# Performance work log

Measured on AMD Instinct MI355X. Metric: run time of the kernel, lower is better.

## Reference

```python
import jax, jax.numpy as jnp
import numpy as np
import math

N_NODES = 20000
N_EDGES = 320000
NODE_IN = 128
HIDDEN = 64
HEADS = 4
TIME_DIM = 64
SCALE = 60.0 / 1.0  # sensitivity / epsilon


def _linear_params(key, din, dout):
    k1, k2 = jax.random.split(key)
    bound = 1.0 / math.sqrt(din)
    w = jax.random.uniform(k1, (din, dout), minval=-bound, maxval=bound, dtype=jnp.float32)
    b = jax.random.uniform(k2, (dout,), minval=-bound, maxval=bound, dtype=jnp.float32)
    return w, b


def setup_inputs() -> dict:
    key = jax.random.key(0)
    ks = jax.random.split(key, 16)
    edge_index = jax.random.randint(ks[0], (2, N_EDGES), 0, N_NODES, dtype=jnp.int64)
    raw_time = jax.random.uniform(ks[1], (N_EDGES, 1), dtype=jnp.float32) * 86400.0
    noise = jax.random.laplace(ks[2], (N_EDGES, 1), dtype=jnp.float32) * SCALE
    node_emb = jax.random.normal(ks[3], (N_NODES, NODE_IN), dtype=jnp.float32)
    HC = HEADS * HIDDEN
    wq1, bq1 = _linear_params(ks[4], NODE_IN, HC)
    wk1, bk1 = _linear_params(ks[5], NODE_IN, HC)
    wv1, bv1 = _linear_params(ks[6], NODE_IN, HC)
    wt1, bt1 = _linear_params(ks[7], TIME_DIM, HC)
    wq2, bq2 = _linear_params(ks[8], HC, HC)
    wk2, bk2 = _linear_params(ks[9], HC, HC)
    wv2, bv2 = _linear_params(ks[10], HC, HC)
    wt2, bt2 = _linear_params(ks[11], TIME_DIM, HC)
    wc, bc = _linear_params(ks[12], HC, 1)
    return dict(edge_index=edge_index, raw_time=raw_time, noise=noise, node_emb=node_emb,
                wq1=wq1, bq1=bq1, wk1=wk1, bk1=bk1, wv1=wv1, bv1=bv1, wt1=wt1, bt1=bt1,
                wq2=wq2, bq2=bq2, wk2=wk2, bk2=bk2, wv2=wv2, bv2=bv2, wt2=wt2, bt2=bt2,
                wc=wc, bc=bc)


def time_encode(t):
    # t: [E, 1] -> [E, TIME_DIM]; interleaved sin/cos as in TimeEncoder
    half = jnp.arange(0, TIME_DIM, 2, dtype=jnp.float32)
    div_term = jnp.exp(half * (-math.log(10000.0) / TIME_DIM))  # [TIME_DIM/2]
    arg = t * div_term  # [E, TIME_DIM/2]
    te = jnp.stack([jnp.sin(arg), jnp.cos(arg)], axis=-1)  # [E, T/2, 2]
    return te.reshape(t.shape[0], TIME_DIM)


def temporal_conv(x, src, dst, time_enc, wq, bq, wk, bk, wv, bv, wt, bt):
    # gather-QKV, edge softmax over dst segments, scatter-add aggregation
    N = x.shape[0]
    q = (x @ wq + bq).reshape(N, HEADS, HIDDEN)
    k = (x @ wk + bk).reshape(N, HEADS, HIDDEN)
    v = (x @ wv + bv).reshape(N, HEADS, HIDDEN)
    t_enc = (time_enc @ wt + bt).reshape(-1, HEADS, HIDDEN)  # [E,H,C]
    q_i = q[dst]                      # [E,H,C]
    k_j = k[src] + t_enc              # [E,H,C]
    alpha = (q_i * k_j).sum(-1) / math.sqrt(HIDDEN)  # [E,H]
    # segment softmax over index = dst (PyG softmax semantics)
    amax = jax.ops.segment_max(alpha, dst, num_segments=N)  # [N,H]
    ea = jnp.exp(alpha - amax[dst])
    denom = jax.ops.segment_sum(ea, dst, num_segments=N)
    alpha = ea / (denom[dst] + 1e-16)
    msg = v[src] * alpha[..., None]   # [E,H,C]
    out = jax.ops.segment_sum(msg, dst, num_segments=N)  # [N,H,C]
    return out.reshape(N, HEADS * HIDDEN)


def reference(edge_index, raw_time, noise, node_emb,
              wq1, bq1, wk1, bk1, wv1, bv1, wt1, bt1,
              wq2, bq2, wk2, bk2, wv2, bv2, wt2, bt2,
              wc, bc):
    src, dst = edge_index[0], edge_index[1]
    noisy_time = raw_time + noise                 # Laplace mechanism
    time_encoded = time_encode(noisy_time)        # [E, TIME_DIM]
    x = jax.nn.relu(temporal_conv(node_emb, src, dst, time_encoded,
                                  wq1, bq1, wk1, bk1, wv1, bv1, wt1, bt1))
    x = jax.nn.relu(temporal_conv(x, src, dst, time_encoded,
                                  wq2, bq2, wk2, bk2, wv2, bv2, wt2, bt2))
    edge_emb = x[src] + x[dst]                    # [E, H*C]
    out = edge_emb @ wc + bc                      # [E, 1]
    return out.squeeze(-1)
```

## Files before the change

kernel.cpp:

```cpp
#include <hip/hip_runtime.h>
#include <hip/hip_fp16.h>
#include <math.h>

#define NN   20000
#define NE   320000
#define NIN  128
#define HC   256
#define NB   1024

typedef unsigned short u16;
typedef __attribute__((ext_vector_type(8))) short bf16x8;
typedef __attribute__((ext_vector_type(8))) unsigned short u16x8;
typedef __attribute__((ext_vector_type(4))) float f32x4;

__device__ __forceinline__ float bf2f(u16 u) {
  union { unsigned int i; float f; } x;
  x.i = ((unsigned int)u) << 16;
  return x.f;
}
__device__ __forceinline__ u16 f2bf(float f) {
  union { float f; unsigned int i; } x;
  x.f = f;
  unsigned int r = x.i + 0x7fffu + ((x.i >> 16) & 1u);
  return (u16)(r >> 16);
}

__device__ __forceinline__ float ldf(const void* p, int i, bool fbf) {
  return fbf ? bf2f(((const u16*)p)[i]) : ((const float*)p)[i];
}
__device__ __forceinline__ int ldsrc(const void* p, int e, bool is64) {
  const int* p32 = (const int*)p;
  return is64 ? p32[2 * e] : p32[e];
}
__device__ __forceinline__ int lddst(const void* p, int e, bool is64) {
  const int* p32 = (const int*)p;
  return is64 ? p32[2 * (NE + e)] : p32[NE + e];
}
__device__ __forceinline__ void stout(void* p, int i, float v, bool fbf) {
  if (fbf) ((u16*)p)[i] = f2bf(v);
  else ((float*)p)[i] = v;
}

__device__ __forceinline__ void gload_lds16(const u16* g, u16* l) {
  __builtin_amdgcn_global_load_lds(
      (const __attribute__((address_space(1))) void*)g,
      (__attribute__((address_space(3))) void*)l, 16, 0, 0);
}

__global__ void devinit_kernel(const void* __restrict__ eidx,
                               const void* __restrict__ nemb,
                               int* __restrict__ flags, float* __restrict__ divt) {
  int lane = threadIdx.x;
  if (lane < 32) {
    const float c32 = (float)(-0.14391156831212787);
    float prod = (float)(2 * lane) * c32;
    divt[lane] = (float)exp((double)prod);
  }
  if (lane == 0) {
    const int* p32 = (const int*)eidx;
    int is64 = 1;
    for (int i = 1; i < 128; i += 2)
      if (p32[i] != 0) { is64 = 0; break; }
    const u16* q16 = (const u16*)nemb;
    int fbf = 1;
    for (int i = 0; i < 128; i += 2) {
      unsigned e = (q16[i] >> 7) & 0xFF;
      if (e < 90 || e > 140) { fbf = 0; break; }
    }
    flags[0] = is64;
    flags[1] = fbf;
  }
}

__global__ void sentinel_kernel(const int* __restrict__ flags, void* __restrict__ out) {
  int i = blockIdx.x * 256 + threadIdx.x;
  if (i < NE) stout(out, i, 3000.0f, flags[1] != 0);
}
__global__ void raw_sentinel_kernel(u16* __restrict__ out) {
  int i = blockIdx.x * 256 + threadIdx.x;
  if (i < NE) out[i] = f2bf(3000.0f);
}

__global__ void zero_kernel(int* __restrict__ p, int n) {
  int i = blockIdx.x * 256 + threadIdx.x;
  if (i < n) p[i] = 0;
}

__global__ void hist_kernel(const int* __restrict__ flags, const void* __restrict__ eidx,
                            int* __restrict__ cnt) {
  bool is64 = flags[0] != 0;
  int e = blockIdx.x * 256 + threadIdx.x;
  if (e < NE) {
    int d = lddst(eidx, e, is64);
    if ((unsigned)d < NN) atomicAdd(&cnt[d], 1);
  }
}

__global__ void scan1_kernel(const int* __restrict__ cnt, int* __restrict__ offs,
                             int* __restrict__ bsum, int n) {
  __shared__ int s[256];
  int b = blockIdx.x, t = threadIdx.x, i = b * 256 + t;
  int x = (i < n) ? cnt[i] : 0;
  s[t] = x;
  __syncthreads();
  for (int off = 1; off < 256; off <<= 1) {
    int y = (t >= off) ? s[t - off] : 0;
    __syncthreads();
    s[t] += y;
    __syncthreads();
  }
  if (i < n) offs[i] = s[t] - x;
  if (t == 255) bsum[b] = s[t];
}

__global__ void scan2_kernel(int* __restrict__ bsum, int* __restrict__ offs,
                             int nb, int n) {
  __shared__ int s[256];
  int t = threadIdx.x;
  int x = (t < nb) ? bsum[t] : 0;
  s[t] = x;
  __syncthreads();
  for (int off = 1; off < 256; off <<= 1) {
    int y = (t >= off) ? s[t - off] : 0;
    __syncthreads();
    s[t] += y;
    __syncthreads();
  }
  if (t < nb) bsum[t] = s[t] - x;
  if (t == 255) offs[n] = s[t];
}

__global__ void scan3_kernel(int* __restrict__ offs, const int* __restrict__ bsum,
                             int* __restrict__ cursor, int n) {
  int i = blockIdx.x * 256 + threadIdx.x;
  if (i < n) {
    int v = offs[i] + bsum[blockIdx.x];
    offs[i] = v;
    cursor[i] = v;
  }
}

__global__ void fill_kernel(const int* __restrict__ flags, const void* __restrict__ eidx,
                            const void* __restrict__ rawt, const void* __restrict__ noise,
                            int* __restrict__ cursor, int* __restrict__ ssrc,
                            float* __restrict__ stt) {
  bool is64 = flags[0] != 0, fbf = flags[1] != 0;
  int e = blockIdx.x * 256 + threadIdx.x;
  if (e < NE) {
    int d = lddst(eidx, e, is64);
    if ((unsigned)d < NN) {
      int pos = atomicAdd(&cursor[d], 1);
      if ((unsigned)pos < NE) {
        int src = ldsrc(eidx, e, is64);
        if ((unsigned)src >= NN) src = 0;
        ssrc[pos] = src;
        stt[pos] = ldf(rawt, e, fbf) + ldf(noise, e, fbf);
      }
    }
  }
}

__global__ __launch_bounds__(256) void te_kernel(
    const float* __restrict__ stt, const float* __restrict__ divt,
    u16* __restrict__ te_s) {
  int idx = blockIdx.x * 256 + threadIdx.x;
  int p = idx >> 5;
  if (p >= NE) return;
  int f = idx & 31;
  float tt = stt[p];
  float arg = tt * divt[f];
  double rev = (double)arg * 0.15915494309189535;
  double fr = rev - floor(rev);
  float red = (float)(fr * 6.283185307179586);
  float sv, cv;
  sincosf(red, &sv, &cv);
  __half hs = __float2half(sv), hc = __float2half(cv);
  unsigned int packed = (unsigned int)(*(u16*)&hs) | ((unsigned int)(*(u16*)&hc) << 16);
  ((unsigned int*)te_s)[(size_t)p * 32 + f] = packed;
}

__global__ void transw3_kernel(const int* __restrict__ flags, const void* __restrict__ W0,
                               const void* __restrict__ W1, const void* __restrict__ W2,
                               u16* __restrict__ WtBig, int K) {
  bool fbf = flags[1] != 0;
  __shared__ u16 tile[64][65];
  int z = blockIdx.z;
  const void* W = (z == 0) ? W0 : (z == 1) ? W1 : W2;
  u16* dst = WtBig + (size_t)z * 256 * K;
  int kb = blockIdx.x * 64, cb = blockIdx.y * 64;
  int tx = threadIdx.x & 63, ty = threadIdx.x >> 6;
  for (int i = ty; i < 64; i += 4)
    tile[tx][i] = f2bf(ldf(W, (kb + i) * HC + cb + tx, fbf));
  __syncthreads();
  for (int i = ty; i < 64; i += 4)
    dst[(size_t)(cb + i) * K + kb + tx] = tile[i][tx];
}

__global__ void wcombbias_kernel(const int* __restrict__ flags, const void* __restrict__ wt,
                                 const u16* __restrict__ Wqt, u16* __restrict__ Wout,
                                 const void* __restrict__ bq, const void* __restrict__ bk,
                                 const void* __restrict__ bv, float* __restrict__ biasBig,
                                 int K) {
  bool fbf = flags[1] != 0;
  int b = blockIdx.x, t = threadIdx.x;
  if (b < 256) {
    __shared__ float wrow[64];
    int j = b, h = j >> 6;
    if (t < 64) wrow[t] = ldf(wt, (j & 63) * HC + h * 64 + t, fbf);
    __syncthreads();
    if (t < K) {
      float s = 0.f;
#pragma unroll 8
      for (int mm = 0; mm < 64; ++mm)
        s += wrow[mm] * bf2f(Wqt[(size_t)(h * 64 + mm) * K + t]);
      Wout[(size_t)j * K + t] = f2bf(s);
    }
  } else if (b < 259) {
    int bb = b - 256;
    const void* p = (bb == 0) ? bq : (bb == 1) ? bk : bv;
    biasBig[bb * 256 + t] = ldf(p, t, fbf);
  } else {
    int j = t, h = j >> 6;
    float s = 0.f;
    for (int mm = 0; mm < 64; ++mm)
      s += ldf(bq, h * 64 + mm, fbf) * ldf(wt, (j & 63) * HC + h * 64 + mm, fbf);
    biasBig[768 + j] = s;
  }
}

template <bool AWS>
__global__ __launch_bounds__(256) void gemm_mfma(
    const int* __restrict__ flags, const void* __restrict__ Ap,
    const u16* __restrict__ Wt, const float* __restrict__ bias,
    u16* __restrict__ C, int M, int K) {
  bool fbf = flags[1] != 0;
  __shared__ u16 As[64 * 32];
  __shared__ u16 Bs[64 * 32];
  int tid = threadIdx.x;
  int rb = blockIdx.x * 64, cb = blockIdx.y * 64;
  int wave = tid >> 6, lane = tid & 63;
  int l15 = lane & 15, quad = lane >> 4;

  f32x4 acc[4];
#pragma unroll
  for (int mt = 0; mt < 4; ++mt)
#pragma unroll
    for (int r = 0; r < 4; ++r) acc[mt][r] = 0.f;

  int srow = tid >> 2;
  int schunk = tid & 3;
  int gchunk = schunk ^ (srow & 3);
  int arow = rb + srow; if (arow >= M) arow = M - 1;
  u16* asl = &As[srow * 32 + schunk * 8];
  u16* bsl = &Bs[srow * 32 + schunk * 8];
  const u16* bsrc = Wt + (size_t)(cb + srow) * K + gchunk * 8;
  const bool adirect = AWS || fbf;
  const u16* asrc = adirect ? ((const u16*)Ap + (size_t)arow * K + gchunk * 8) : (const u16*)0;

  for (int kk = 0; kk < K; kk += 32) {
    if (adirect) {
      gload_lds16(asrc + kk, asl);
    } else {
      const float* A = (const float*)Ap + (size_t)arow * K + kk + gchunk * 8;
      bf16x8 tmp;
#pragma unroll
      for (int i = 0; i < 8; ++i) tmp[i] = (short)f2bf(A[i]);
      *(bf16x8*)asl = tmp;
    }
    gload_lds16(bsrc + kk, bsl);
    __syncthreads();

    int bcol = wave * 16 + l15;
    bf16x8 bfrag = *(const bf16x8*)&Bs[bcol * 32 + ((quad ^ (bcol & 3)) * 8)];
#pragma unroll
    for (int mt = 0; mt < 4; ++mt) {
      int ar = mt * 16 + l15;
      bf16x8 afrag = *(const bf16x8*)&As[ar * 32 + ((quad ^ (ar & 3)) * 8)];
      acc[mt] = __builtin_amdgcn_mfma_f32_16x16x32_bf16(afrag, bfrag, acc[mt], 0, 0, 0);
    }
    __syncthreads();
  }

  int gcol = cb + wave * 16 + l15;
  float bv = bias[gcol];
  int scol;
  if (gcol < 256) scol = gcol;
  else if (gcol < 512) { int cc = gcol - 256; scol = 256 + ((cc >> 2) << 3) + (cc & 3); }
  else if (gcol < 768) { int cc = gcol - 512; scol = 256 + ((cc >> 2) << 3) + 4 + (cc & 3); }
  else scol = gcol;
#pragma unroll
  for (int mt = 0; mt < 4; ++mt) {
#pragma unroll
    for (int r = 0; r < 4; ++r) {
      int grow = rb + mt * 16 + quad * 4 + r;
      if (grow < M) C[(size_t)grow * NB + scol] = f2bf(acc[mt][r] + bv);
    }
  }
}

template <int DOY>
__global__ __launch_bounds__(256) void aggfused_kernel(
    const int* __restrict__ flags, const int* __restrict__ ssrc,
    const int* __restrict__ offsets, const u16* __restrict__ te_s,
    const u16* __restrict__ qkvp, const void* __restrict__ bt,
    u16* __restrict__ xout, const void* __restrict__ wc,
    float* __restrict__ ynode) {
  bool fbf = flags[1] != 0;
  int w = threadIdx.x >> 6;
  int n = blockIdx.x * 4 + w;
  if (n >= NN) return;
  int lane = threadIdx.x & 63;
  int c = lane * 4;
  int s0 = offsets[n], s1 = offsets[n + 1];
  if (s0 < 0) s0 = 0;
  if (s1 > NE) s1 = NE;

  ushort4 q4 = *(const ushort4*)(qkvp + (size_t)n * NB + c);
  ushort4 p4 = *(const ushort4*)(qkvp + (size_t)n * NB + 768 + c);
  float qx = bf2f(q4.x), qy = bf2f(q4.y), qz = bf2f(q4.z), qw = bf2f(q4.w);
  float px = bf2f(p4.x), py = bf2f(p4.y), pz = bf2f(p4.z), pw = bf2f(p4.w);
  float pb = qx * ldf(bt, c + 0, fbf);
  pb += qy * ldf(bt, c + 1, fbf);
  pb += qz * ldf(bt, c + 2, fbf);
  pb += qw * ldf(bt, c + 3, fbf);
  pb += __shfl_xor(pb, 1);
  pb += __shfl_xor(pb, 2);
  pb += __shfl_xor(pb, 4);
  pb += __shfl_xor(pb, 8);
  float qb = pb;
  int jb = c & 63;
  int kvoff = 256 + lane * 8;

  float m = -INFINITY, denom = 0.f;
  float acc0 = 0.f, acc1 = 0.f, acc2 = 0.f, acc3 = 0.f;

#define ALPHA_OF(kv, t4, out_a, okflag)                                        \
  {                                                                            \
    float s = qx * bf2f((kv)[0]) + __half2float(*(__half*)&(t4).x) * px;       \
    s += qy * bf2f((kv)[1]) + __half2float(*(__half*)&(t4).y) * py;            \
    s += qz * bf2f((kv)[2]) + __half2float(*(__half*)&(t4).z) * pz;            \
    s += qw * bf2f((kv)[3]) + __half2float(*(__half*)&(t4).w) * pw;            \
    s += __shfl_xor(s, 1);                                                     \
    s += __shfl_xor(s, 2);                                                     \
    s += __shfl_xor(s, 4);                                                     \
    s += __shfl_xor(s, 8);                                                     \
    out_a = (okflag) ? (s + qb) * 0.125f : 0.f;                                \
  }

#define STATE_UPDATE(a, kv, okflag)                                            \
  {                                                                            \
    float ea;                                                                  \
    if ((a) > m) {                                                             \
      float sc = __expf(m - (a));                                              \
      denom *= sc;                                                             \
      acc0 *= sc; acc1 *= sc; acc2 *= sc; acc3 *= sc;                          \
      m = (a);                                                                 \
      ea = 1.0f;                                                               \
    } else {                                                                   \
      ea = __expf((a) - m);                                                    \
    }                                                                          \
    denom += ea;                                                               \
    if (okflag) {                                                              \
      acc0 += ea * bf2f((kv)[4]);                                              \
      acc1 += ea * bf2f((kv)[5]);                                              \
      acc2 += ea * bf2f((kv)[6]);                                              \
      acc3 += ea * bf2f((kv)[7]);                                              \
    }                                                                          \
  }

  int p = s0;
  for (; p + 3 < s1; p += 4) {
    int srcA = ssrc[p], srcB = ssrc[p + 1], srcC = ssrc[p + 2], srcD = ssrc[p + 3];
    bool okA = (unsigned)srcA < NN, okB = (unsigned)srcB < NN;
    bool okC = (unsigned)srcC < NN, okD = (unsigned)srcD < NN;
    if (!okA) srcA = 0;
    if (!okB) srcB = 0;
    if (!okC) srcC = 0;
    if (!okD) srcD = 0;
    u16x8 kvA = *(const u16x8*)(qkvp + (size_t)srcA * NB + kvoff);
    u16x8 kvB = *(const u16x8*)(qkvp + (size_t)srcB * NB + kvoff);
    u16x8 kvC = *(const u16x8*)(qkvp + (size_t)srcC * NB + kvoff);
    u16x8 kvD = *(const u16x8*)(qkvp + (size_t)srcD * NB + kvoff);
    ushort4 tA = *(const ushort4*)(te_s + (size_t)p * 64 + jb);
    ushort4 tB = *(const ushort4*)(te_s + (size_t)(p + 1) * 64 + jb);
    ushort4 tC = *(const ushort4*)(te_s + (size_t)(p + 2) * 64 + jb);
    ushort4 tD = *(const ushort4*)(te_s + (size_t)(p + 3) * 64 + jb);

    float aA, aB, aC, aD;
    ALPHA_OF(kvA, tA, aA, okA)
    ALPHA_OF(kvB, tB, aB, okB)
    ALPHA_OF(kvC, tC, aC, okC)
    ALPHA_OF(kvD, tD, aD, okD)
    STATE_UPDATE(aA, kvA, okA)
    STATE_UPDATE(aB, kvB, okB)
    STATE_UPDATE(aC, kvC, okC)
    STATE_UPDATE(aD, kvD, okD)
  }
  for (; p < s1; ++p) {
    int src = ssrc[p];
    bool ok = (unsigned)src < NN;
    if (!ok) src = 0;
    u16x8 kv = *(const u16x8*)(qkvp + (size_t)src * NB + kvoff);
    ushort4 t4 = *(const ushort4*)(te_s + (size_t)p * 64 + jb);
    float a;
    ALPHA_OF(kv, t4, a, ok)
    STATE_UPDATE(a, kv, ok)
  }
#undef ALPHA_OF
#undef STATE_UPDATE

  float inv = 1.f / (denom + 1e-16f);
  ushort4 r;
  r.x = f2bf(fmaxf(acc0 * inv, 0.f));
  r.y = f2bf(fmaxf(acc1 * inv, 0.f));
  r.z = f2bf(fmaxf(acc2 * inv, 0.f));
  r.w = f2bf(fmaxf(acc3 * inv, 0.f));
  *(ushort4*)(xout + (size_t)n * HC + c) = r;
  if (DOY) {
    float yv = bf2f(r.x) * ldf(wc, c + 0, fbf);
    yv += bf2f(r.y) * ldf(wc, c + 1, fbf);
    yv += bf2f(r.z) * ldf(wc, c + 2, fbf);
    yv += bf2f(r.w) * ldf(wc, c + 3, fbf);
    for (int off = 32; off; off >>= 1) yv += __shfl_xor(yv, off);
    if (lane == 0) ynode[n] = yv;
  }
}

__global__ __launch_bounds__(256) void final2_kernel(
    const int* __restrict__ flags, const void* __restrict__ eidx,
    const float* __restrict__ y, const void* __restrict__ bc,
    void* __restrict__ out) {
  bool is64 = flags[0] != 0, fbf = flags[1] != 0;
  int e = blockIdx.x * 256 + threadIdx.x;
  if (e >= NE) return;
  int src = ldsrc(eidx, e, is64);
  int dst = lddst(eidx, e, is64);
  if ((unsigned)src >= NN) src = 0;
  if ((unsigned)dst >= NN) dst = 0;
  stout(out, e, y[src] + y[dst] + ldf(bc, 0, fbf), fbf);
}

extern "C" void kernel_launch(void* const* d_in, const int* in_sizes, int n_in,
                              void* d_out, int out_size, void* d_ws, size_t ws_size,
                              hipStream_t stream) {
  const void* eidx  = d_in[0];
  const void* rawt  = d_in[1];
  const void* noise = d_in[2];
  const void* nemb  = d_in[3];
  const void *wq1 = d_in[4],  *bq1 = d_in[5];
  const void *wk1 = d_in[6],  *bk1 = d_in[7];
  const void *wv1 = d_in[8],  *bv1 = d_in[9];
  const void *wt1 = d_in[10], *bt1 = d_in[11];
  const void *wq2 = d_in[12], *bq2 = d_in[13];
  const void *wk2 = d_in[14], *bk2 = d_in[15];
  const void *wv2 = d_in[16], *bv2 = d_in[17];
  const void *wt2 = d_in[18], *bt2 = d_in[19];
  const void *wcp = d_in[20], *bcp = d_in[21];

  char* ws = (char*)d_ws;
  size_t off = 0;
  auto alloc = [&](size_t bytes) -> void* {
    void* p = ws + off;
    off += (bytes + 255) & ~(size_t)255;
    return p;
  };
  int*   flags  = (int*)alloc(256);
  float* divt   = (float*)alloc(256);
  u16*   WtBig  = (u16*)alloc((size_t)NB * HC * 2);
  float* biasBig= (float*)alloc((size_t)NB * 4);
  u16*   qkvp   = (u16*)alloc((size_t)NN * NB * 2);
  u16*   x1     = (u16*)alloc((size_t)NN * HC * 2);
  u16*   x2     = (u16*)alloc((size_t)NN * HC * 2);
  float* ynode  = (float*)alloc((size_t)NN * 4);
  int* offsets  = (int*)alloc((size_t)(NN + 1) * 4);
  int* cursor   = (int*)alloc((size_t)NN * 4);
  int* bsum     = (int*)alloc(256 * 4);
  int* ssrc     = (int*)alloc((size_t)NE * 4);
  float* stt    = (float*)alloc((size_t)NE * 4);
  u16* te_s     = (u16*)alloc((size_t)NE * 64 * 2);
  size_t need = off;

  int gN = (NN + 255) / 256, gE = (NE + 255) / 256;
  int nb = (NN + 255) / 256;

  if (ws_size < 1024) {
    raw_sentinel_kernel<<<gE, 256, 0, stream>>>((u16*)d_out);
    return;
  }
  devinit_kernel<<<1, 64, 0, stream>>>(eidx, nemb, flags, divt);
  if (need > ws_size) {
    sentinel_kernel<<<gE, 256, 0, stream>>>(flags, d_out);
    return;
  }

  zero_kernel<<<gN, 256, 0, stream>>>(cursor, NN);
  hist_kernel<<<gE, 256, 0, stream>>>(flags, eidx, cursor);
  scan1_kernel<<<nb, 256, 0, stream>>>(cursor, offsets, bsum, NN);
  scan2_kernel<<<1, 256, 0, stream>>>(bsum, offsets, nb, NN);
  scan3_kernel<<<nb, 256, 0, stream>>>(offsets, bsum, cursor, NN);
  fill_kernel<<<gE, 256, 0, stream>>>(flags, eidx, rawt, noise, cursor, ssrc, stt);

  int gTe = (NE * 32 + 255) / 256;
  te_kernel<<<gTe, 256, 0, stream>>>(stt, divt, te_s);

  dim3 ggemm((NN + 63) / 64, NB / 64);
  dim3 gt1(NIN / 64, 4, 3), gt2(HC / 64, 4, 3);
  int gNode = (NN + 3) / 4;

  transw3_kernel<<<gt1, 256, 0, stream>>>(flags, wq1, wk1, wv1, WtBig, NIN);
  wcombbias_kernel<<<260, 256, 0, stream>>>(flags, wt1, WtBig, WtBig + (size_t)768 * NIN,
                                            bq1, bk1, bv1, biasBig, NIN);
  gemm_mfma<false><<<ggemm, 256, 0, stream>>>(flags, nemb, WtBig, biasBig, qkvp, NN, NIN);
  aggfused_kernel<0><<<gNode, 256, 0, stream>>>(flags, ssrc, offsets, te_s, qkvp, bt1,
                                                x1, wcp, ynode);

  transw3_kernel<<<gt2, 256, 0, stream>>>(flags, wq2, wk2, wv2, WtBig, HC);
  wcombbias_kernel<<<260, 256, 0, stream>>>(flags, wt2, WtBig, WtBig + (size_t)768 * HC,
                                            bq2, bk2, bv2, biasBig, HC);
  gemm_mfma<true><<<ggemm, 256, 0, stream>>>(flags, x1, WtBig, biasBig, qkvp, NN, HC);
  aggfused_kernel<1><<<gNode, 256, 0, stream>>>(flags, ssrc, offsets, te_s, qkvp, bt2,
                                                x2, wcp, ynode);

  final2_kernel<<<gE, 256, 0, stream>>>(flags, eidx, ynode, bcp, d_out);
}
```

Before: 394.2 us.

## Enlarge GEMM block tile to 128x128 with 2x2 wave layout and 4x4 MFMA subtiles

The QKV projection GEMM now uses 128x128 output tiles per block. Each of the four waves computes a 64x64 subtile with a 4x4 grid of MFMA accumulators, and B fragments are reused across the M subtiles. This raises arithmetic intensity and cuts LDS and global reloads per MFMA. In exchange it uses more registers, and the grid shrinks to about 157x8 blocks, which lowers occupancy and parallelism.

```diff
diff --git a/kernel.cpp b/kernel.cpp
--- a/kernel.cpp
+++ b/kernel.cpp
@@ -234,66 +234,88 @@
     const u16* __restrict__ Wt, const float* __restrict__ bias,
     u16* __restrict__ C, int M, int K) {
   bool fbf = flags[1] != 0;
-  __shared__ u16 As[64 * 32];
-  __shared__ u16 Bs[64 * 32];
+  __shared__ u16 As[128 * 32];
+  __shared__ u16 Bs[128 * 32];
   int tid = threadIdx.x;
-  int rb = blockIdx.x * 64, cb = blockIdx.y * 64;
+  int rb = blockIdx.x * 128, cb = blockIdx.y * 128;
   int wave = tid >> 6, lane = tid & 63;
   int l15 = lane & 15, quad = lane >> 4;
-
-  f32x4 acc[4];
+  int mbase = (wave >> 1) * 64, nbase = (wave & 1) * 64;
+
+  f32x4 acc[4][4];
 #pragma unroll
   for (int mt = 0; mt < 4; ++mt)
 #pragma unroll
-    for (int r = 0; r < 4; ++r) acc[mt][r] = 0.f;
-
-  int srow = tid >> 2;
-  int schunk = tid & 3;
-  int gchunk = schunk ^ (srow & 3);
-  int arow = rb + srow; if (arow >= M) arow = M - 1;
-  u16* asl = &As[srow * 32 + schunk * 8];
-  u16* bsl = &Bs[srow * 32 + schunk * 8];
-  const u16* bsrc = Wt + (size_t)(cb + srow) * K + gchunk * 8;
+    for (int nt = 0; nt < 4; ++nt)
+#pragma unroll
+      for (int r = 0; r < 4; ++r) acc[mt][nt][r] = 0.f;
+
+  int srow0 = tid >> 2, schunk0 = tid & 3;
+  int srow1 = (tid + 256) >> 2, schunk1 = (tid + 256) & 3;
+  int gchunk0 = schunk0 ^ (srow0 & 3);
+  int gchunk1 = schunk1 ^ (srow1 & 3);
+  int arow0 = rb + srow0; if (arow0 >= M) arow0 = M - 1;
+  int arow1 = rb + srow1; if (arow1 >= M) arow1 = M - 1;
+  u16* asl0 = &As[srow0 * 32 + schunk0 * 8];
+  u16* asl1 = &As[srow1 * 32 + schunk1 * 8];
+  u16* bsl0 = &Bs[srow0 * 32 + schunk0 * 8];
+  u16* bsl1 = &Bs[srow1 * 32 + schunk1 * 8];
+  const u16* bsrc0 = Wt + (size_t)(cb + srow0) * K + gchunk0 * 8;
+  const u16* bsrc1 = Wt + (size_t)(cb + srow1) * K + gchunk1 * 8;
   const bool adirect = AWS || fbf;
-  const u16* asrc = adirect ? ((const u16*)Ap + (size_t)arow * K + gchunk * 8) : (const u16*)0;
+  const u16* asrc0 = adirect ? ((const u16*)Ap + (size_t)arow0 * K + gchunk0 * 8) : (const u16*)0;
+  const u16* asrc1 = adirect ? ((const u16*)Ap + (size_t)arow1 * K + gchunk1 * 8) : (const u16*)0;
 
   for (int kk = 0; kk < K; kk += 32) {
     if (adirect) {
-      gload_lds16(asrc + kk, asl);
+      gload_lds16(asrc0 + kk, asl0);
+      gload_lds16(asrc1 + kk, asl1);
     } else {
-      const float* A = (const float*)Ap + (size_t)arow * K + kk + gchunk * 8;
-      bf16x8 tmp;
-#pragma unroll
-      for (int i = 0; i < 8; ++i) tmp[i] = (short)f2bf(A[i]);
-      *(bf16x8*)asl = tmp;
-    }
-    gload_lds16(bsrc + kk, bsl);
-    __syncthreads();
-
-    int bcol = wave * 16 + l15;
-    bf16x8 bfrag = *(const bf16x8*)&Bs[bcol * 32 + ((quad ^ (bcol & 3)) * 8)];
+      const float* A0 = (const float*)Ap + (size_t)arow0 * K + kk + gchunk0 * 8;
+      const float* A1 = (const float*)Ap + (size_t)arow1 * K + kk + gchunk1 * 8;
+      bf16x8 t0, t1;
+#pragma unroll
+      for (int i = 0; i < 8; ++i) { t0[i] = (short)f2bf(A0[i]); t1[i] = (short)f2bf(A1[i]); }
+      *(bf16x8*)asl0 = t0;
+      *(bf16x8*)asl1 = t1;
+    }
+    gload_lds16(bsrc0 + kk, bsl0);
+    gload_lds16(bsrc1 + kk, bsl1);
+    __syncthreads();
+
+    bf16x8 bfrag[4];
+#pragma unroll
+    for (int nt = 0; nt < 4; ++nt) {
+      int col = nbase + nt * 16 + l15;
+      bfrag[nt] = *(const bf16x8*)&Bs[col * 32 + ((quad ^ (col & 3)) * 8)];
+    }
 #pragma unroll
     for (int mt = 0; mt < 4; ++mt) {
-      int ar = mt * 16 + l15;
-      bf16x8 afrag = *(const bf16x8*)&As[ar * 32 + ((quad ^ (ar & 3)) * 8)];
-      acc[mt] = __builtin_amdgcn_mfma_f32_16x16x32_bf16(afrag, bfrag, acc[mt], 0, 0, 0);
-    }
-    __syncthreads();
-  }
-
-  int gcol = cb + wave * 16 + l15;
-  float bv = bias[gcol];
-  int scol;
-  if (gcol < 256) scol = gcol;
-  else if (gcol < 512) { int cc = gcol - 256; scol = 256 + ((cc >> 2) << 3) + (cc & 3); }
-  else if (gcol < 768) { int cc = gcol - 512; scol = 256 + ((cc >> 2) << 3) + 4 + (cc & 3); }
-  else scol = gcol;
-#pragma unroll
-  for (int mt = 0; mt < 4; ++mt) {
-#pragma unroll
-    for (int r = 0; r < 4; ++r) {
-      int grow = rb + mt * 16 + quad * 4 + r;
-      if (grow < M) C[(size_t)grow * NB + scol] = f2bf(acc[mt][r] + bv);
+      int row = mbase + mt * 16 + l15;
+      bf16x8 afrag = *(const bf16x8*)&As[row * 32 + ((quad ^ (row & 3)) * 8)];
+#pragma unroll
+      for (int nt = 0; nt < 4; ++nt)
+        acc[mt][nt] = __builtin_amdgcn_mfma_f32_16x16x32_bf16(afrag, bfrag[nt], acc[mt][nt], 0, 0, 0);
+    }
+    __syncthreads();
+  }
+
+#pragma unroll
+  for (int nt = 0; nt < 4; ++nt) {
+    int gcol = cb + nbase + nt * 16 + l15;
+    float bv = bias[gcol];
+    int scol;
+    if (gcol < 256) scol = gcol;
+    else if (gcol < 512) { int cc = gcol - 256; scol = 256 + ((cc >> 2) << 3) + (cc & 3); }
+    else if (gcol < 768) { int cc = gcol - 512; scol = 256 + ((cc >> 2) << 3) + 4 + (cc & 3); }
+    else scol = gcol;
+#pragma unroll
+    for (int mt = 0; mt < 4; ++mt) {
+#pragma unroll
+      for (int r = 0; r < 4; ++r) {
+        int grow = rb + mbase + mt * 16 + quad * 4 + r;
+        if (grow < M) C[(size_t)grow * NB + scol] = f2bf(acc[mt][nt][r] + bv);
+      }
     }
   }
 }
@@ -503,7 +525,7 @@
   int gTe = (NE * 32 + 255) / 256;
   te_kernel<<<gTe, 256, 0, stream>>>(stt, divt, te_s);
 
-  dim3 ggemm((NN + 63) / 64, NB / 64);
+  dim3 ggemm((NN + 127) / 128, NB / 128);
   dim3 gt1(NIN / 64, 4, 3), gt2(HC / 64, 4, 3);
   int gNode = (NN + 3) / 4;
 
```

New measurement: 393.8 us. No clear change (-0.1%).
